# Performance work log

Hardware: AMD Instinct MI355X
Metric: run time of the kernel (lower is better)

The kernel has to match this reference:

```python
import jax, jax.numpy as jnp
import numpy as np
from jax import lax

GAMMA = 1.0       # SoftDTW gamma (init default)
MAX_DIST = 10000.0  # clamp in SoftDTW.forward
# bandwidth=None -> 0 -> Sakoe-Chiba pruning disabled (condition 0 < bandwidth never holds)


def _softdtw(D, gamma):
    """Soft-DTW DP via anti-diagonal wavefront scan. D: (B, N, M) -> (B,)."""
    B, N, M = D.shape
    R = jnp.full((B, N + 2, M + 2), jnp.inf, D.dtype).at[:, 0, 0].set(0.0)
    i_vec = jnp.arange(1, N + 1)  # row indices of interior cells

    def step(R, p):
        # cells on anti-diagonal p satisfy i + j == p + 2
        j_vec = p + 2 - i_vec
        valid = (j_vec >= 1) & (j_vec <= M)
        jc = jnp.clip(j_vec, 1, M)
        r0 = R[:, i_vec - 1, jc - 1]  # (B, N) diag
        r1 = R[:, i_vec - 1, jc]      # up
        r2 = R[:, i_vec, jc - 1]      # left
        neg = jnp.stack([r0, r1, r2], axis=0) * (-1.0 / gamma)  # (3, B, N)
        # invalid lanes: keep finite to avoid NaNs (result discarded by where)
        neg = jnp.where(valid[None, None, :], neg, 0.0)
        softmin = -gamma * jax.scipy.special.logsumexp(neg, axis=0)  # (B, N)
        new = D[:, i_vec - 1, jc - 1] + softmin
        R = R.at[:, i_vec, jc].set(jnp.where(valid[None, :], new, R[:, i_vec, jc]))
        return R, None

    R, _ = lax.scan(step, R, jnp.arange(N + M - 1))
    return R[:, N, M]


def setup_inputs() -> dict:
    key = jax.random.key(0)
    kx, ky = jax.random.split(key)
    X = jax.random.normal(kx, (16, 512, 64), dtype=jnp.float32)
    Y = jax.random.normal(ky, (16, 512, 64), dtype=jnp.float32)
    return {"X": X, "Y": Y}


def reference(X, Y):
    # squared Euclidean pairwise distance per timestep (faithful expand form)
    D = jnp.sum((X[:, :, None, :] - Y[:, None, :, :]) ** 2, axis=-1)  # (B, N, M)
    D = jnp.minimum(D, MAX_DIST)
    return _softdtw(D, GAMMA)
```

## Files before the change

### kernel.cpp

```cpp
#include <hip/hip_runtime.h>

#define BIGF 1e30f
#define LOG2E 1.4426950408889634f
#define LN2F 0.6931471805599453f

constexpr int NB = 16;
constexpr int NN = 512;
constexpr int MM = 512;
constexpr int KD = 64;
constexpr int WAVES = 8;
constexpr int CSPAN = 32;
constexpr int NSPANS = 32;
constexpr int SPW = 18;
constexpr int TPH = 3 * (WAVES - 1) + SPW;
constexpr int DIAGELEMS = NN * MM;

constexpr int BBSTRIDE = 672;
constexpr int BUFD_FLOATS = WAVES * 2 * CSPAN * 64;
constexpr int BBUF_FLOATS = WAVES * BBSTRIDE;
constexpr int SMEM_BYTES = (BUFD_FLOATS + BBUF_FLOATS) * 4;

__device__ __forceinline__ int Bclosed(int s) {
  return (s <= 511) ? (s * (s + 1)) / 2
                    : DIAGELEMS - ((1023 - s) * (1024 - s)) / 2 - (s - 511);
}

__global__ __launch_bounds__(256) void pairdist_kernel(
    const float* __restrict__ X, const float* __restrict__ Y,
    float* __restrict__ Dsk) {
  const int b = blockIdx.z;
  const int i0 = blockIdx.y * 64;
  const int j0 = blockIdx.x * 64;

  __shared__ float Xs[64][65];
  __shared__ float Ys[64][65];
  __shared__ float Ds[64][66];

  const float* Xb = X + ((size_t)b * NN + i0) * KD;
  const float* Yb = Y + ((size_t)b * MM + j0) * KD;
  for (int k = threadIdx.x; k < 64 * KD; k += 256) {
    Xs[k >> 6][k & 63] = Xb[k];
    Ys[k >> 6][k & 63] = Yb[k];
  }
  __syncthreads();

  const int tx = threadIdx.x & 15;
  const int ty = threadIdx.x >> 4;
  const int r0 = ty * 4, c0 = tx * 4;

  float acc[4][4];
#pragma unroll
  for (int a = 0; a < 4; ++a)
#pragma unroll
    for (int e = 0; e < 4; ++e) acc[a][e] = 0.0f;

  for (int d = 0; d < KD; ++d) {
    float xv[4], yv[4];
#pragma unroll
    for (int q = 0; q < 4; ++q) xv[q] = Xs[r0 + q][d];
#pragma unroll
    for (int q = 0; q < 4; ++q) yv[q] = Ys[c0 + q][d];
#pragma unroll
    for (int a = 0; a < 4; ++a)
#pragma unroll
      for (int e = 0; e < 4; ++e) {
        float df = xv[a] - yv[e];
        acc[a][e] = fmaf(df, df, acc[a][e]);
      }
  }

#pragma unroll
  for (int a = 0; a < 4; ++a)
#pragma unroll
    for (int e = 0; e < 4; ++e)
      Ds[r0 + a][c0 + e] = fminf(acc[a][e], 10000.0f) * LOG2E;
  __syncthreads();

  const int wv = threadIdx.x >> 6;
  const int ln = threadIdx.x & 63;
  float* Db = Dsk + (size_t)b * DIAGELEMS;
  for (int sl = wv; sl < 127; sl += 4) {
    const int istart = sl > 63 ? sl - 63 : 0;
    const int iend = sl < 63 ? sl : 63;
    if (ln <= iend - istart) {
      const int ig = i0 + istart + ln;
      Db[Bclosed(i0 + j0 + sl) + ig] = Ds[istart + ln][sl - istart - ln];
    }
  }
}

__device__ __forceinline__ float dpp_shr1_old(float oldv, float v) {
  return __int_as_float(__builtin_amdgcn_update_dpp(
      __float_as_int(oldv), __float_as_int(v), 0x138 , 0xf, 0xf,
      false));
}
__device__ __forceinline__ float dpp_shl1(float v) {
  return __int_as_float(__builtin_amdgcn_update_dpp(
      __float_as_int(v), __float_as_int(v), 0x130 , 0xf, 0xf,
      false));
}

__device__ __forceinline__ void dma_span(const float* __restrict__ Dskb,
                                         float* bufD, int blk, int q,
                                         int lane) {
  float* dst0 = bufD + (blk * 2 + (q & 1)) * (CSPAN * 64);
  const int rbase = 64 * blk + (lane & 15) * 4;
  const int sub = lane >> 4;
#pragma unroll
  for (int u = 0; u < 8; ++u) {
    int s = 32 * q + 4 * u + sub;
    s = s > 1022 ? 1022 : s;
    int e = Bclosed(s) + rbase;
    e = e > DIAGELEMS - 4 ? DIAGELEMS - 4 : e;
    __builtin_amdgcn_global_load_lds(
        (const __attribute__((address_space(1))) void*)(Dskb + e),
        (__attribute__((address_space(3))) void*)(dst0 + u * 256), 16, 0, 0);
  }
}

#define SOFTMIN_STEP(K)                                                     \
  {                                                                         \
    const float up1 = dpp_shr1_old(B, ra);                                  \
    B = dpp_shl1(B);                                                        \
    const float m = fminf(fminf(up1, up2), ra);                             \
    const float md = __builtin_amdgcn_fmed3f(up1, up2, ra);                 \
    const float mx = fmaxf(fmaxf(up1, up2), ra);                            \
    const float ssum = (__builtin_amdgcn_exp2f(m - md) +                    \
                        __builtin_amdgcn_exp2f(m - mx)) +                   \
                       1.0f;                                                \
    n = dv[K] + (m - __builtin_amdgcn_logf(ssum));                          \
    up2 = up1;                                                              \
  }

extern __shared__ float smem[];
__global__ __launch_bounds__(512) void softdtw_kernel(
    const float* __restrict__ Dsk, float* __restrict__ out) {
  const int b = blockIdx.x;
  const int t = threadIdx.x;
  const int wu = __builtin_amdgcn_readfirstlane(t >> 6);
  const int lane = t & 63;
  const int blk = ((wu & 3) << 1) | (wu >> 2);

  float* bufD = smem;
  float* bbuf = smem + BUFD_FLOATS;

  for (int k = t; k < BBUF_FLOATS; k += 512) bbuf[k] = BIGF;
  __syncthreads();

  const float* __restrict__ Dskb = Dsk + (size_t)b * DIAGELEMS;

  dma_span(Dskb, bufD, blk, 2 * blk, lane);

  const int r = 64 * blk + lane;
  float ra = BIGF;
  float up2 = (blk == 0 && lane == 0) ? 0.0f : BIGF;

  for (int S = 0; S < TPH; ++S) {
    const int cc = S - 3 * blk;
    if (cc >= 0 && cc < SPW) {
      const int c = cc + 2 * blk;
      if (cc + 1 < SPW) {
        dma_span(Dskb, bufD, blk, c + 1, lane);
        asm volatile("s_waitcnt vmcnt(8)" ::: "memory");
      } else {
        asm volatile("s_waitcnt vmcnt(0)" ::: "memory");
      }

      float B = BIGF;
      if (blk) B = bbuf[blk * BBSTRIDE + 62 + 32 * cc + 1 + lane];

      const float* myD = bufD + (blk * 2 + (c & 1)) * (CSPAN * 64);
      const __attribute__((address_space(3))) float* mp =
          (const __attribute__((address_space(3))) float*)(myD + lane);
      unsigned maddr = (unsigned)(size_t)mp;

      float dv[CSPAN];
      asm volatile(
          "ds_read_b32 %0, %32 offset:0\n\t"
          "ds_read_b32 %1, %32 offset:256\n\t"
          "ds_read_b32 %2, %32 offset:512\n\t"
          "ds_read_b32 %3, %32 offset:768\n\t"
          "ds_read_b32 %4, %32 offset:1024\n\t"
          "ds_read_b32 %5, %32 offset:1280\n\t"
          "ds_read_b32 %6, %32 offset:1536\n\t"
          "ds_read_b32 %7, %32 offset:1792\n\t"
          "ds_read_b32 %8, %32 offset:2048\n\t"
          "ds_read_b32 %9, %32 offset:2304\n\t"
          "ds_read_b32 %10, %32 offset:2560\n\t"
          "ds_read_b32 %11, %32 offset:2816\n\t"
          "ds_read_b32 %12, %32 offset:3072\n\t"
          "ds_read_b32 %13, %32 offset:3328\n\t"
          "ds_read_b32 %14, %32 offset:3584\n\t"
          "ds_read_b32 %15, %32 offset:3840\n\t"
          "ds_read_b32 %16, %32 offset:4096\n\t"
          "ds_read_b32 %17, %32 offset:4352\n\t"
          "ds_read_b32 %18, %32 offset:4608\n\t"
          "ds_read_b32 %19, %32 offset:4864\n\t"
          "ds_read_b32 %20, %32 offset:5120\n\t"
          "ds_read_b32 %21, %32 offset:5376\n\t"
          "ds_read_b32 %22, %32 offset:5632\n\t"
          "ds_read_b32 %23, %32 offset:5888\n\t"
          "ds_read_b32 %24, %32 offset:6144\n\t"
          "ds_read_b32 %25, %32 offset:6400\n\t"
          "ds_read_b32 %26, %32 offset:6656\n\t"
          "ds_read_b32 %27, %32 offset:6912\n\t"
          "ds_read_b32 %28, %32 offset:7168\n\t"
          "ds_read_b32 %29, %32 offset:7424\n\t"
          "ds_read_b32 %30, %32 offset:7680\n\t"
          "ds_read_b32 %31, %32 offset:7936\n\t"
          "s_waitcnt lgkmcnt(0)"
          : "=&v"(dv[0]), "=&v"(dv[1]), "=&v"(dv[2]), "=&v"(dv[3]),
            "=&v"(dv[4]), "=&v"(dv[5]), "=&v"(dv[6]), "=&v"(dv[7]),
            "=&v"(dv[8]), "=&v"(dv[9]), "=&v"(dv[10]), "=&v"(dv[11]),
            "=&v"(dv[12]), "=&v"(dv[13]), "=&v"(dv[14]), "=&v"(dv[15]),
            "=&v"(dv[16]), "=&v"(dv[17]), "=&v"(dv[18]), "=&v"(dv[19]),
            "=&v"(dv[20]), "=&v"(dv[21]), "=&v"(dv[22]), "=&v"(dv[23]),
            "=&v"(dv[24]), "=&v"(dv[25]), "=&v"(dv[26]), "=&v"(dv[27]),
            "=&v"(dv[28]), "=&v"(dv[29]), "=&v"(dv[30]), "=&v"(dv[31])
          : "v"(maddr)
          : "memory");

      float* pubp =
          bbuf + ((blk + 1) & 7) * BBSTRIDE + (62 + 32 * c - r + 1);

      float n;
      if (cc >= 2 && cc <= 15) {
#pragma unroll
        for (int k = 0; k < CSPAN; ++k) {
          SOFTMIN_STEP(k);
          ra = n;
          pubp[k] = ra;
        }
      } else {
        const int jv0 = 32 * c - r + 1;
#pragma unroll
        for (int k = 0; k < CSPAN; ++k) {
          SOFTMIN_STEP(k);
          const bool a0 = (unsigned)(jv0 + k - 1) < (unsigned)MM;
          ra = a0 ? n : ra;
          pubp[k] = ra;
        }
      }
    }
    __syncthreads();
  }

  if (blk == WAVES - 1 && lane == 63) out[b] = ra * LN2F;
}

extern "C" void kernel_launch(void* const* d_in, const int* in_sizes, int n_in,
                              void* d_out, int out_size, void* d_ws,
                              size_t ws_size, hipStream_t stream) {
  const float* X = (const float*)d_in[0];
  const float* Y = (const float*)d_in[1];
  float* out = (float*)d_out;
  float* Dsk = (float*)d_ws;

  const size_t needed = (size_t)NB * DIAGELEMS * sizeof(float);
  if (ws_size < needed) return;

  hipFuncSetAttribute((const void*)softdtw_kernel,
                      hipFuncAttributeMaxDynamicSharedMemorySize, SMEM_BYTES);

  pairdist_kernel<<<dim3(MM / 64, NN / 64, NB), 256, 0, stream>>>(X, Y, Dsk);
  softdtw_kernel<<<NB, 512, SMEM_BYTES, stream>>>(Dsk, out);
}
```

Baseline: 132.3 us.

## Replace float log-sum-exp recurrence with custom 12-bit log-domain integer arithmetic

Re-encodes each cost cell as exp(-D) in a packed integer format: an exponent in the high bits and a 12-bit mantissa. The soft-min step then becomes integer shifts, an add, a 24-bit multiply and a count-leading-zeros normalisation instead of exp2 and log transcendentals on the serial critical path. The pairwise-distance kernel precomputes the encoding, and a single log is applied at the end. The cost is a loss of precision: 12-bit mantissas with truncating shifts only approximate the float soft-DTW recurrence, and error can accumulate across 1023 diagonals.

```diff
diff --git a/kernel.cpp b/kernel.cpp
--- a/kernel.cpp
+++ b/kernel.cpp
@@ -1,6 +1,5 @@
 #include <hip/hip_runtime.h>
 
-#define BIGF 1e30f
 #define LOG2E 1.4426950408889634f
 #define LN2F 0.6931471805599453f
 
@@ -14,11 +13,13 @@
 constexpr int SPW = 18;
 constexpr int TPH = 3 * (WAVES - 1) + SPW;
 constexpr int DIAGELEMS = NN * MM;
+constexpr int EMIN = -(1 << 18);
+#define PINF ((int)((unsigned)EMIN << 12))
 
 constexpr int BBSTRIDE = 672;
-constexpr int BUFD_FLOATS = WAVES * 2 * CSPAN * 64;
-constexpr int BBUF_FLOATS = WAVES * BBSTRIDE;
-constexpr int SMEM_BYTES = (BUFD_FLOATS + BBUF_FLOATS) * 4;
+constexpr int BUFD_U32 = WAVES * 2 * CSPAN * 64;
+constexpr int BBUF_U32 = WAVES * BBSTRIDE;
+constexpr int SMEM_BYTES = (BUFD_U32 + BBUF_U32) * 4;
 
 __device__ __forceinline__ int Bclosed(int s) {
   return (s <= 511) ? (s * (s + 1)) / 2
@@ -27,14 +28,14 @@
 
 __global__ __launch_bounds__(256) void pairdist_kernel(
     const float* __restrict__ X, const float* __restrict__ Y,
-    float* __restrict__ Dsk) {
+    unsigned* __restrict__ Dsk) {
   const int b = blockIdx.z;
   const int i0 = blockIdx.y * 64;
   const int j0 = blockIdx.x * 64;
 
   __shared__ float Xs[64][65];
   __shared__ float Ys[64][65];
-  __shared__ float Ds[64][66];
+  __shared__ unsigned Ds[64][66];
 
   const float* Xb = X + ((size_t)b * NN + i0) * KD;
   const float* Yb = Y + ((size_t)b * MM + j0) * KD;
@@ -72,13 +73,19 @@
 #pragma unroll
   for (int a = 0; a < 4; ++a)
 #pragma unroll
-    for (int e = 0; e < 4; ++e)
-      Ds[r0 + a][c0 + e] = fminf(acc[a][e], 10000.0f) * LOG2E;
+    for (int e = 0; e < 4; ++e) {
+      const float Dp = fminf(acc[a][e], 10000.0f) * LOG2E;
+      const float ef = floorf(Dp);
+      const float mt = __builtin_amdgcn_exp2f(ef - Dp);
+      const unsigned mut = min(4095u, (unsigned)(mt * 4096.0f));
+      const int et = -(int)ef;
+      Ds[r0 + a][c0 + e] = ((unsigned)et << 12) | mut;
+    }
   __syncthreads();
 
   const int wv = threadIdx.x >> 6;
   const int ln = threadIdx.x & 63;
-  float* Db = Dsk + (size_t)b * DIAGELEMS;
+  unsigned* Db = Dsk + (size_t)b * DIAGELEMS;
   for (int sl = wv; sl < 127; sl += 4) {
     const int istart = sl > 63 ? sl - 63 : 0;
     const int iend = sl < 63 ? sl : 63;
@@ -89,21 +96,17 @@
   }
 }
 
-__device__ __forceinline__ float dpp_shr1_old(float oldv, float v) {
-  return __int_as_float(__builtin_amdgcn_update_dpp(
-      __float_as_int(oldv), __float_as_int(v), 0x138 , 0xf, 0xf,
-      false));
-}
-__device__ __forceinline__ float dpp_shl1(float v) {
-  return __int_as_float(__builtin_amdgcn_update_dpp(
-      __float_as_int(v), __float_as_int(v), 0x130 , 0xf, 0xf,
-      false));
-}
-
-__device__ __forceinline__ void dma_span(const float* __restrict__ Dskb,
-                                         float* bufD, int blk, int q,
+__device__ __forceinline__ int dpp_shr1_old_i(int oldv, int v) {
+  return __builtin_amdgcn_update_dpp(oldv, v, 0x138, 0xf, 0xf, false);
+}
+__device__ __forceinline__ int dpp_shl1_i(int v) {
+  return __builtin_amdgcn_update_dpp(v, v, 0x130, 0xf, 0xf, false);
+}
+
+__device__ __forceinline__ void dma_span(const unsigned* __restrict__ Dskb,
+                                         unsigned* bufD, int blk, int q,
                                          int lane) {
-  float* dst0 = bufD + (blk * 2 + (q & 1)) * (CSPAN * 64);
+  unsigned* dst0 = bufD + (blk * 2 + (q & 1)) * (CSPAN * 64);
   const int rbase = 64 * blk + (lane & 15) * 4;
   const int sub = lane >> 4;
 #pragma unroll
@@ -118,42 +121,55 @@
   }
 }
 
-#define SOFTMIN_STEP(K)                                                     \
+#define SOFTMIN_STEP(PK)                                                    \
   {                                                                         \
-    const float up1 = dpp_shr1_old(B, ra);                                  \
-    B = dpp_shl1(B);                                                        \
-    const float m = fminf(fminf(up1, up2), ra);                             \
-    const float md = __builtin_amdgcn_fmed3f(up1, up2, ra);                 \
-    const float mx = fmaxf(fmaxf(up1, up2), ra);                            \
-    const float ssum = (__builtin_amdgcn_exp2f(m - md) +                    \
-                        __builtin_amdgcn_exp2f(m - mx)) +                   \
-                       1.0f;                                                \
-    n = dv[K] + (m - __builtin_amdgcn_logf(ssum));                          \
-    up2 = up1;                                                              \
-  }
-
-extern __shared__ float smem[];
+    const int up1P = dpp_shr1_old_i(B, P);           \
+    B = dpp_shl1_i(B);                                                      \
+    const int e1 = up1P >> 12;                                              \
+    const unsigned mu1 = (unsigned)up1P & 4095u;                            \
+    const int emax = max(max(e1, e2), e0);                                  \
+    const unsigned sh1 = min((unsigned)(emax - e1), 31u);                   \
+    const unsigned sh2 = min((unsigned)(emax - e2), 31u);                   \
+    const unsigned sh0 = min((unsigned)(emax - e0), 31u);                   \
+    const unsigned ssum = (mu1 >> sh1) + (mu2 >> sh2) + (mu0 >> sh0);       \
+    const int et = ((int)(PK)) >> 12;                                       \
+    const unsigned mut = (PK)&4095u;                                        \
+    const unsigned prod = __umul24(ssum, mut);     \
+    const int lz = __builtin_clz(prod | 1u);                                \
+    nmu = prod >> (unsigned)(20 - lz);        \
+    ne = emax + et + (8 - lz);                                              \
+    nP = (int)(((unsigned)ne << 12) + nmu);                                 \
+    e2 = e1;                                                                \
+    mu2 = mu1;                                                              \
+  }
+
+extern __shared__ unsigned usmem[];
 __global__ __launch_bounds__(512) void softdtw_kernel(
-    const float* __restrict__ Dsk, float* __restrict__ out) {
+    const unsigned* __restrict__ Dsk, float* __restrict__ out) {
   const int b = blockIdx.x;
   const int t = threadIdx.x;
   const int wu = __builtin_amdgcn_readfirstlane(t >> 6);
   const int lane = t & 63;
   const int blk = ((wu & 3) << 1) | (wu >> 2);
 
-  float* bufD = smem;
-  float* bbuf = smem + BUFD_FLOATS;
-
-  for (int k = t; k < BBUF_FLOATS; k += 512) bbuf[k] = BIGF;
+  unsigned* bufD = usmem;
+  unsigned* bbuf = usmem + BUFD_U32;
+
+  for (int k = t; k < BBUF_U32; k += 512) bbuf[k] = (unsigned)PINF;
   __syncthreads();
 
-  const float* __restrict__ Dskb = Dsk + (size_t)b * DIAGELEMS;
+  const unsigned* __restrict__ Dskb = Dsk + (size_t)b * DIAGELEMS;
 
   dma_span(Dskb, bufD, blk, 2 * blk, lane);
 
   const int r = 64 * blk + lane;
-  float ra = BIGF;
-  float up2 = (blk == 0 && lane == 0) ? 0.0f : BIGF;
+  int P = PINF;
+  int e0 = EMIN;
+  unsigned mu0 = 0;
+  int e2;
+  unsigned mu2;
+  if (blk == 0 && lane == 0) { e2 = 1; mu2 = 2048; }
+  else { e2 = EMIN; mu2 = 0; }
 
   for (int S = 0; S < TPH; ++S) {
     const int cc = S - 3 * blk;
@@ -166,15 +182,19 @@
         asm volatile("s_waitcnt vmcnt(0)" ::: "memory");
       }
 
-      float B = BIGF;
-      if (blk) B = bbuf[blk * BBSTRIDE + 62 + 32 * cc + 1 + lane];
-
-      const float* myD = bufD + (blk * 2 + (c & 1)) * (CSPAN * 64);
-      const __attribute__((address_space(3))) float* mp =
-          (const __attribute__((address_space(3))) float*)(myD + lane);
+      int B = PINF;
+      if (blk) {
+        int bi = 62 + 32 * cc + 1 + lane;
+        bi = bi > BBSTRIDE - 1 ? BBSTRIDE - 1 : bi;
+        B = (int)bbuf[blk * BBSTRIDE + bi];
+      }
+
+      const unsigned* myD = bufD + (blk * 2 + (c & 1)) * (CSPAN * 64);
+      const __attribute__((address_space(3))) unsigned* mp =
+          (const __attribute__((address_space(3))) unsigned*)(myD + lane);
       unsigned maddr = (unsigned)(size_t)mp;
 
-      float dv[CSPAN];
+      unsigned dv[CSPAN];
       asm volatile(
           "ds_read_b32 %0, %32 offset:0\n\t"
           "ds_read_b32 %1, %32 offset:256\n\t"
@@ -220,32 +240,38 @@
           : "v"(maddr)
           : "memory");
 
-      float* pubp =
+      unsigned* pubp =
           bbuf + ((blk + 1) & 7) * BBSTRIDE + (62 + 32 * c - r + 1);
 
-      float n;
+      int nP, ne;
+      unsigned nmu;
       if (cc >= 2 && cc <= 15) {
 #pragma unroll
         for (int k = 0; k < CSPAN; ++k) {
-          SOFTMIN_STEP(k);
-          ra = n;
-          pubp[k] = ra;
+          SOFTMIN_STEP(dv[k]);
+          P = nP;
+          e0 = ne;
+          mu0 = nmu;
+          pubp[k] = (unsigned)P;
         }
       } else {
         const int jv0 = 32 * c - r + 1;
 #pragma unroll
         for (int k = 0; k < CSPAN; ++k) {
-          SOFTMIN_STEP(k);
+          SOFTMIN_STEP(dv[k]);
           const bool a0 = (unsigned)(jv0 + k - 1) < (unsigned)MM;
-          ra = a0 ? n : ra;
-          pubp[k] = ra;
+          P = a0 ? nP : P;
+          e0 = a0 ? ne : e0;
+          mu0 = a0 ? nmu : mu0;
+          pubp[k] = (unsigned)P;
         }
       }
     }
     __syncthreads();
   }
 
-  if (blk == WAVES - 1 && lane == 63) out[b] = ra * LN2F;
+  if (blk == WAVES - 1 && lane == 63)
+    out[b] = ((float)(12 - e0) - __builtin_amdgcn_logf((float)mu0)) * LN2F;
 }
 
 extern "C" void kernel_launch(void* const* d_in, const int* in_sizes, int n_in,
@@ -254,9 +280,9 @@
   const float* X = (const float*)d_in[0];
   const float* Y = (const float*)d_in[1];
   float* out = (float*)d_out;
-  float* Dsk = (float*)d_ws;
-
-  const size_t needed = (size_t)NB * DIAGELEMS * sizeof(float);
+  unsigned* Dsk = (unsigned*)d_ws;
+
+  const size_t needed = (size_t)NB * DIAGELEMS * sizeof(unsigned);
   if (ws_size < needed) return;
 
   hipFuncSetAttribute((const void*)softdtw_kernel,
```

Result: slower. 165.7 us (+25.3%).
